# Kernel tuning notes

Hardware: AMD Instinct MI355X
Metric: run time of the kernel (lower is better)

## Reference

```python
import jax, jax.numpy as jnp
import numpy as np

N = 28  # hardcoded grid side in the module


def setup_inputs() -> dict:
    key = jax.random.key(0)
    k1, k2, k3 = jax.random.split(key, 3)
    B = 65536
    x = jax.random.normal(k1, (B, N, N), dtype=jnp.float32)
    # intended init: pos2d = meshgrid positions (xy indexing), stacked on last dim
    xx, yy = jnp.meshgrid(jnp.arange(N), jnp.arange(N), indexing='xy')
    pos2d = jnp.stack([xx, yy], axis=-1).astype(jnp.float32)
    pos2d = pos2d + 0.01 * jax.random.normal(k2, (N, N, 2), dtype=jnp.float32)
    weight = jnp.full((N, N), 0.167, dtype=jnp.float32)
    ep = jnp.full((N, N), -0.1, dtype=jnp.float32) + 0.01 * jax.random.normal(k3, (N, N), dtype=jnp.float32)
    return {"x": x, "pos2d": pos2d, "weight": weight, "ep": ep}


def reference(x, pos2d, weight, ep):
    # grid[a, b] = (b, a) per torch.meshgrid(indexing='xy') stacked on dim -1
    xx, yy = jnp.meshgrid(jnp.arange(N), jnp.arange(N), indexing='xy')
    grid = jnp.stack([xx, yy], axis=-1).astype(pos2d.dtype)            # (28, 28, 2)
    # pairwise position deltas: grid index (a,b) vs learned pos2d at (c,d)
    diff = grid[:, :, None, None, :] - pos2d[None, None, :, :, :]       # (28, 28, 28, 28, 2)
    d2 = jnp.sum(diff * diff, axis=-1)                                  # (28, 28, 28, 28)
    valid = (d2 < 9).astype(d2.dtype)                                   # hard cutoff disk
    ep_neg = -jax.nn.relu(-ep)                                          # clamp ep to <= 0, (28, 28) broadcast over last two dims
    w = jnp.exp(ep_neg * d2) * valid                                    # Gaussian decay * mask
    W = w.reshape(N * N, N * N)                                         # (784, 784)
    B = x.shape[0]
    # torch: matmul(W, x_flat.T).T  ==  x_flat @ W.T
    out = (x.reshape(B, N * N) @ W.T).reshape(B, N, N) * weight
    return out
```

## Files before the change

### kernel.cpp

```cpp
#include <hip/hip_runtime.h>
#include <stdint.h>

typedef __attribute__((ext_vector_type(8))) short short8;
typedef __attribute__((ext_vector_type(4))) float f32x4;
typedef __attribute__((ext_vector_type(8))) float f32x8;
typedef __attribute__((ext_vector_type(16))) float f32x16;
typedef __attribute__((ext_vector_type(2))) float f32x2;
typedef __bf16 bf16x8_t __attribute__((ext_vector_type(8)));

#define NN 784
#define NA 28
#define ABYTES 16384
#define NIMG 128
#define OROW 232

__device__ __forceinline__ unsigned short f2bf(float f) {
  unsigned int u = __float_as_uint(f);
  return (unsigned short)((u + 0x7FFFu + ((u >> 16) & 1u)) >> 16);
}

__device__ __forceinline__ short8 cvt8(f32x4 lo, f32x4 hi) {
  f32x8 f = {lo.x, lo.y, lo.z, lo.w, hi.x, hi.y, hi.z, hi.w};
  bf16x8_t b = __builtin_convertvector(f, bf16x8_t);
  return __builtin_bit_cast(short8, b);
}

__host__ __device__ constexpr int slot0c(int a) {
  int t = 28 * a - 84;
  if (t < 0) t = 0;
  t >>= 5;
  if (t > 17) t = 17;
  return t;
}
__host__ __device__ constexpr int tgtc(int I) { int a2 = I + 2 > 27 ? 27 : I + 2; return slot0c(a2) + 7; }
__host__ __device__ constexpr bool xissue(int I) { return I >= 1 && tgtc(I) > tgtc(I - 1); }
__host__ __device__ constexpr bool xcvt(int A)   { return A >= 3 && xissue(A - 2); }

__global__ void build_w_kernel(const float* __restrict__ pos2d,
                               const float* __restrict__ weight,
                               const float* __restrict__ ep,
                               unsigned short* __restrict__ Bpack) {
  int idx = blockIdx.x * 256 + threadIdx.x;
  int u    = idx & 511;
  int frag = idx >> 9;
  int s2 = frag & 15;
  int a  = frag >> 4;
  int j    = u & 7;
  int lane = u >> 3;
  int outcol = lane & 31;
  int kh     = lane >> 5;
  int kk = kh * 8 + j;
  int kglob = slot0c(a) * 32 + s2 * 16 + kk;
  float val = 0.f;
  if (outcol < 28 && kglob < NN) {
    float px = pos2d[2 * kglob + 0];
    float py = pos2d[2 * kglob + 1];
    float dx = (float)outcol - px;
    float dy = (float)a - py;
    float d2 = __fadd_rn(__fmul_rn(dx, dx), __fmul_rn(dy, dy));
    if (d2 < 9.0f) {
      float en = fminf(ep[kglob], 0.f);
      val = expf(en * d2) * weight[a * 28 + outcol];
    }
  }
  Bpack[idx] = f2bf(val);
}

template <int A>
struct It {
  static __device__ __forceinline__ void run(
      const float* __restrict__ xrow, const unsigned short* __restrict__ Bpack,
      char* __restrict__ wlds, char* __restrict__ olds,
      float* __restrict__ oblk, int tid, int lane,
      short8 (&rlo)[10], short8 (&rhi)[10], f32x4 (&stg)[2][4]) {
    constexpr int T0 = slot0c(A);
    const int il = lane & 31;
    const int kh = lane >> 5;

    f32x4 sr[4];
    if constexpr (A + 1 < NA) {
      const char* src = (const char*)Bpack + (A + 1) * ABYTES + tid * 16;
      #pragma unroll
      for (int r = 0; r < 4; ++r)
        sr[r] = *(const f32x4*)(src + r * 4096);
    }

    if constexpr (xcvt(A)) {
      constexpr int S = slot0c(A) + 7;
      rlo[S % 10] = cvt8(stg[A & 1][0], stg[A & 1][1]);
      if constexpr (S < 24) rhi[S % 10] = cvt8(stg[A & 1][2], stg[A & 1][3]);
      else                  rhi[S % 10] = short8{};
    }
    if constexpr (xissue(A)) {
      constexpr int S = tgtc(A);
      const float* p = xrow + S * 32 + kh * 8;
      stg[A & 1][0] = *(const f32x4*)p;
      stg[A & 1][1] = *(const f32x4*)(p + 4);
      if constexpr (S < 24) {
        stg[A & 1][2] = *(const f32x4*)(p + 16);
        stg[A & 1][3] = *(const f32x4*)(p + 20);
      }
    }

    const char* wbuf = wlds + (A % 3) * ABYTES + lane * 16;
    f32x16 acc = {};
#define KSTEP(s) { constexpr int SL = (T0 + ((s) >> 1)) % 10;                   \
    short8 wf = *(const short8*)(wbuf + (s) * 1024);                            \
    acc = __builtin_amdgcn_mfma_f32_32x32x16_bf16(                              \
        wf, ((s) & 1) ? rhi[SL] : rlo[SL], acc, 0, 0, 0); }
    KSTEP(0)  KSTEP(1)  KSTEP(2)  KSTEP(3)
    KSTEP(4)  KSTEP(5)  KSTEP(6)  KSTEP(7)
    KSTEP(8)  KSTEP(9)  KSTEP(10) KSTEP(11)
    KSTEP(12) KSTEP(13) KSTEP(14) KSTEP(15)
#undef KSTEP

    if constexpr (A + 1 < NA) {
      char* dst = wlds + ((A + 1) % 3) * ABYTES + tid * 16;
      #pragma unroll
      for (int r = 0; r < 4; ++r)
        *(f32x4*)(dst + r * 4096) = sr[r];
    }

    {
      char* obase = olds + (tid >> 6) * 32 * OROW + il * OROW + ((A & 1) * 28 + 4 * kh) * 4;
      #pragma unroll
      for (int g = 0; g < 4; ++g) {
        if (g < 3 || kh == 0) {
          f32x2 v0 = {acc[4 * g + 0], acc[4 * g + 1]};
          f32x2 v1 = {acc[4 * g + 2], acc[4 * g + 3]};
          *(f32x2*)(obase + g * 32) = v0;
          *(f32x2*)(obase + g * 32 + 8) = v1;
        }
      }
    }

    __builtin_amdgcn_s_barrier();

    if constexpr (A & 1) {
      constexpr int P = A >> 1;
      #pragma unroll
      for (int r = 0; r < 14; ++r) {
        int e = r * 256 + tid;
        int img = e / 28, u = e - img * 28;
        f32x2 v = *(const f32x2*)(olds + img * OROW + u * 8);
        *(f32x2*)((char*)(oblk + (size_t)img * NN + P * 56) + u * 8) = v;
      }
      __builtin_amdgcn_s_barrier();
    }

    It<A + 1>::run(xrow, Bpack, wlds, olds, oblk, tid, lane, rlo, rhi, stg);
  }
};
template <>
struct It<NA> {
  static __device__ __forceinline__ void run(const float*, const unsigned short*,
                                             char*, char*, float*, int, int,
                                             short8 (&)[10], short8 (&)[10],
                                             f32x4 (&)[2][4]) {}
};

__global__ __launch_bounds__(256, 2)
void gemm_kernel(const float* __restrict__ x,
                 const unsigned short* __restrict__ Bpack,
                 float* __restrict__ out) {
  __shared__ char wlds[3 * ABYTES];
  __shared__ char olds[NIMG * OROW];

  const int tid  = threadIdx.x;
  const int wave = tid >> 6;
  const int lane = tid & 63;
  const int il   = lane & 31;
  const int kh   = lane >> 5;
  const int m0   = blockIdx.x * NIMG + wave * 32;

  const float* xrow = x + (size_t)(m0 + il) * NN;
  float*       oblk = out + (size_t)(blockIdx.x * NIMG) * NN;

  short8 rlo[10], rhi[10];
  f32x4  stg[2][4];

  {
    const char* src = (const char*)Bpack + tid * 16;
    #pragma unroll
    for (int r = 0; r < 4; ++r) {
      f32x4 v = *(const f32x4*)(src + r * 4096);
      *(f32x4*)(wlds + tid * 16 + r * 4096) = v;
    }
  }

#define PRO(S) { const float* p = xrow + (S) * 32 + kh * 8;                     \
    f32x4 a0 = *(const f32x4*)p,        a1 = *(const f32x4*)(p + 4);            \
    f32x4 b0 = *(const f32x4*)(p + 16), b1 = *(const f32x4*)(p + 20);           \
    rlo[S] = cvt8(a0, a1); rhi[S] = cvt8(b0, b1); }
  PRO(0) PRO(1) PRO(2) PRO(3) PRO(4) PRO(5) PRO(6) PRO(7)
#undef PRO

  __syncthreads();

  It<0>::run(xrow, Bpack, wlds, olds, oblk, tid, lane, rlo, rhi, stg);
}

extern "C" void kernel_launch(void* const* d_in, const int* in_sizes, int n_in,
                              void* d_out, int out_size, void* d_ws, size_t ws_size,
                              hipStream_t stream) {
  const float* x      = (const float*)d_in[0];
  const float* pos2d  = (const float*)d_in[1];
  const float* weight = (const float*)d_in[2];
  const float* ep     = (const float*)d_in[3];
  float* out          = (float*)d_out;
  unsigned short* Bpack = (unsigned short*)d_ws;

  int batch = in_sizes[0] / NN;

  build_w_kernel<<<dim3((NA * 16 * 512) / 256), dim3(256), 0, stream>>>(
      pos2d, weight, ep, Bpack);
  gemm_kernel<<<dim3(batch / NIMG), dim3(256), 0, stream>>>(x, Bpack, out);
}
```

Baseline: 124.4 us.

## Deepen prefetch pipelines and double-buffer output staging to drop extra barriers

The weight-tile prefetch now runs two iterations ahead through a double-buffered register set, and the x-row staging runs three iterations ahead across 12 register slots. Output staging moves to two LDS buffers, each holding one row-block. The store of the previous row-block to global memory is issued before the current block is written to LDS, which removes the second barrier per pair of iterations. MFMA sections also get raised wave priority, and the prologue interleaves loads with conversions. The cost is more live registers under launch_bounds(256,2), which risks spills or lower occupancy.

```diff
diff --git a/kernel.cpp b/kernel.cpp
--- a/kernel.cpp
+++ b/kernel.cpp
@@ -5,14 +5,13 @@
 typedef __attribute__((ext_vector_type(4))) float f32x4;
 typedef __attribute__((ext_vector_type(8))) float f32x8;
 typedef __attribute__((ext_vector_type(16))) float f32x16;
-typedef __attribute__((ext_vector_type(2))) float f32x2;
 typedef __bf16 bf16x8_t __attribute__((ext_vector_type(8)));
 
 #define NN 784
 #define NA 28
 #define ABYTES 16384
 #define NIMG 128
-#define OROW 232
+#define OT 14336
 
 __device__ __forceinline__ unsigned short f2bf(float f) {
   unsigned int u = __float_as_uint(f);
@@ -32,9 +31,9 @@
   if (t > 17) t = 17;
   return t;
 }
-__host__ __device__ constexpr int tgtc(int I) { int a2 = I + 2 > 27 ? 27 : I + 2; return slot0c(a2) + 7; }
-__host__ __device__ constexpr bool xissue(int I) { return I >= 1 && tgtc(I) > tgtc(I - 1); }
-__host__ __device__ constexpr bool xcvt(int A)   { return A >= 3 && xissue(A - 2); }
+__host__ __device__ constexpr int tgt3(int I) { int a2 = I + 3 > 27 ? 27 : I + 3; return slot0c(a2) + 7; }
+__host__ __device__ constexpr bool xiss(int I) { return I >= 1 && tgt3(I) > tgt3(I - 1); }
+__host__ __device__ constexpr bool xcv(int A)  { return A >= 4 && xiss(A - 3); }
 
 __global__ void build_w_kernel(const float* __restrict__ pos2d,
                                const float* __restrict__ weight,
@@ -72,39 +71,39 @@
       const float* __restrict__ xrow, const unsigned short* __restrict__ Bpack,
       char* __restrict__ wlds, char* __restrict__ olds,
       float* __restrict__ oblk, int tid, int lane,
-      short8 (&rlo)[10], short8 (&rhi)[10], f32x4 (&stg)[2][4]) {
+      short8 (&rlo)[12], short8 (&rhi)[12],
+      f32x4 (&stg)[3][4], f32x4 (&sr)[2][4]) {
     constexpr int T0 = slot0c(A);
     const int il = lane & 31;
     const int kh = lane >> 5;
 
-    f32x4 sr[4];
-    if constexpr (A + 1 < NA) {
-      const char* src = (const char*)Bpack + (A + 1) * ABYTES + tid * 16;
+    if constexpr (A + 2 < NA) {
+      const char* src = (const char*)Bpack + (A + 2) * ABYTES + tid * 16;
       #pragma unroll
       for (int r = 0; r < 4; ++r)
-        sr[r] = *(const f32x4*)(src + r * 4096);
-    }
-
-    if constexpr (xcvt(A)) {
-      constexpr int S = slot0c(A) + 7;
-      rlo[S % 10] = cvt8(stg[A & 1][0], stg[A & 1][1]);
-      if constexpr (S < 24) rhi[S % 10] = cvt8(stg[A & 1][2], stg[A & 1][3]);
-      else                  rhi[S % 10] = short8{};
-    }
-    if constexpr (xissue(A)) {
-      constexpr int S = tgtc(A);
+        sr[A & 1][r] = *(const f32x4*)(src + r * 4096);
+    }
+    if constexpr (xcv(A)) {
+      constexpr int S = tgt3(A - 3);
+      rlo[S % 12] = cvt8(stg[A % 3][0], stg[A % 3][1]);
+      if constexpr (S < 24) rhi[S % 12] = cvt8(stg[A % 3][2], stg[A % 3][3]);
+      else                  rhi[S % 12] = short8{};
+    }
+    if constexpr (xiss(A)) {
+      constexpr int S = tgt3(A);
       const float* p = xrow + S * 32 + kh * 8;
-      stg[A & 1][0] = *(const f32x4*)p;
-      stg[A & 1][1] = *(const f32x4*)(p + 4);
+      stg[A % 3][0] = *(const f32x4*)p;
+      stg[A % 3][1] = *(const f32x4*)(p + 4);
       if constexpr (S < 24) {
-        stg[A & 1][2] = *(const f32x4*)(p + 16);
-        stg[A & 1][3] = *(const f32x4*)(p + 20);
+        stg[A % 3][2] = *(const f32x4*)(p + 16);
+        stg[A % 3][3] = *(const f32x4*)(p + 20);
       }
     }
 
     const char* wbuf = wlds + (A % 3) * ABYTES + lane * 16;
     f32x16 acc = {};
-#define KSTEP(s) { constexpr int SL = (T0 + ((s) >> 1)) % 10;                   \
+    __builtin_amdgcn_s_setprio(1);
+#define KSTEP(s) { constexpr int SL = (T0 + ((s) >> 1)) % 12;                   \
     short8 wf = *(const short8*)(wbuf + (s) * 1024);                            \
     acc = __builtin_amdgcn_mfma_f32_32x32x16_bf16(                              \
         wf, ((s) & 1) ? rhi[SL] : rlo[SL], acc, 0, 0, 0); }
@@ -113,91 +112,110 @@
     KSTEP(8)  KSTEP(9)  KSTEP(10) KSTEP(11)
     KSTEP(12) KSTEP(13) KSTEP(14) KSTEP(15)
 #undef KSTEP
+    __builtin_amdgcn_s_setprio(0);
 
     if constexpr (A + 1 < NA) {
       char* dst = wlds + ((A + 1) % 3) * ABYTES + tid * 16;
       #pragma unroll
       for (int r = 0; r < 4; ++r)
-        *(f32x4*)(dst + r * 4096) = sr[r];
-    }
-
-    {
-      char* obase = olds + (tid >> 6) * 32 * OROW + il * OROW + ((A & 1) * 28 + 4 * kh) * 4;
-      #pragma unroll
-      for (int g = 0; g < 4; ++g) {
-        if (g < 3 || kh == 0) {
-          f32x2 v0 = {acc[4 * g + 0], acc[4 * g + 1]};
-          f32x2 v1 = {acc[4 * g + 2], acc[4 * g + 3]};
-          *(f32x2*)(obase + g * 32) = v0;
-          *(f32x2*)(obase + g * 32 + 8) = v1;
+        *(f32x4*)(dst + r * 4096) = sr[(A + 1) & 1][r];
+    }
+
+    if constexpr (A >= 1) {
+      constexpr int P = A - 1;
+      const char* src = olds + (P & 1) * OT;
+      #pragma unroll
+      for (int r = 0; r < 4; ++r) {
+        int e = r * 256 + tid;
+        if (r < 3 || e < 896) {
+          int img = e / 7, u = e - img * 7;
+          f32x4 v = *(const f32x4*)(src + img * 112 + u * 16);
+          *(f32x4*)(oblk + (size_t)img * NN + P * 28 + u * 4) = v;
         }
       }
     }
 
+    {
+      char* ob = olds + (A & 1) * OT + ((tid >> 6) * 32 + il) * 112 + kh * 16;
+      #pragma unroll
+      for (int g = 0; g < 4; ++g)
+        if (g < 3 || kh == 0) {
+          f32x4 v = {acc[4 * g + 0], acc[4 * g + 1], acc[4 * g + 2], acc[4 * g + 3]};
+          *(f32x4*)(ob + g * 32) = v;
+        }
+    }
+
     __builtin_amdgcn_s_barrier();
-
-    if constexpr (A & 1) {
-      constexpr int P = A >> 1;
-      #pragma unroll
-      for (int r = 0; r < 14; ++r) {
-        int e = r * 256 + tid;
-        int img = e / 28, u = e - img * 28;
-        f32x2 v = *(const f32x2*)(olds + img * OROW + u * 8);
-        *(f32x2*)((char*)(oblk + (size_t)img * NN + P * 56) + u * 8) = v;
-      }
-      __builtin_amdgcn_s_barrier();
-    }
-
-    It<A + 1>::run(xrow, Bpack, wlds, olds, oblk, tid, lane, rlo, rhi, stg);
+    It<A + 1>::run(xrow, Bpack, wlds, olds, oblk, tid, lane, rlo, rhi, stg, sr);
   }
 };
 template <>
 struct It<NA> {
   static __device__ __forceinline__ void run(const float*, const unsigned short*,
                                              char*, char*, float*, int, int,
-                                             short8 (&)[10], short8 (&)[10],
-                                             f32x4 (&)[2][4]) {}
+                                             short8 (&)[12], short8 (&)[12],
+                                             f32x4 (&)[3][4], f32x4 (&)[2][4]) {}
 };
 
 __global__ __launch_bounds__(256, 2)
 void gemm_kernel(const float* __restrict__ x,
                  const unsigned short* __restrict__ Bpack,
                  float* __restrict__ out) {
-  __shared__ char wlds[3 * ABYTES];
-  __shared__ char olds[NIMG * OROW];
+  __shared__ __align__(16) char wlds[3 * ABYTES];
+  __shared__ __align__(16) char olds[2 * OT];
 
   const int tid  = threadIdx.x;
   const int wave = tid >> 6;
   const int lane = tid & 63;
   const int il   = lane & 31;
   const int kh   = lane >> 5;
-  const int m0   = blockIdx.x * NIMG + wave * 32;
-
-  const float* xrow = x + (size_t)(m0 + il) * NN;
+
+  const float* xrow = x + (size_t)(blockIdx.x * NIMG + wave * 32 + il) * NN;
   float*       oblk = out + (size_t)(blockIdx.x * NIMG) * NN;
 
-  short8 rlo[10], rhi[10];
-  f32x4  stg[2][4];
+  short8 rlo[12], rhi[12];
+  f32x4  stg[3][4], sr[2][4];
+
+  const char* bsrc = (const char*)Bpack + tid * 16;
+  f32x4 w0r[4];
+  #pragma unroll
+  for (int r = 0; r < 4; ++r)
+    w0r[r] = *(const f32x4*)(bsrc + r * 4096);
+
+#define PLOAD(S) { const float* p = xrow + (S) * 32 + kh * 8;                   \
+    stg[(S) % 3][0] = *(const f32x4*)p;       stg[(S) % 3][1] = *(const f32x4*)(p + 4);  \
+    stg[(S) % 3][2] = *(const f32x4*)(p + 16); stg[(S) % 3][3] = *(const f32x4*)(p + 20); }
+#define PCVT(S)  { rlo[S] = cvt8(stg[(S) % 3][0], stg[(S) % 3][1]);             \
+                   rhi[S] = cvt8(stg[(S) % 3][2], stg[(S) % 3][3]); }
+  PLOAD(0) PLOAD(1) PCVT(0) PLOAD(2) PCVT(1) PLOAD(3) PCVT(2)
+  PLOAD(4) PCVT(3)  PLOAD(5) PCVT(4) PLOAD(6) PCVT(5) PLOAD(7) PCVT(6) PCVT(7)
+#undef PLOAD
+#undef PCVT
+
+  #pragma unroll
+  for (int r = 0; r < 4; ++r)
+    sr[1][r] = *(const f32x4*)(bsrc + ABYTES + r * 4096);
+
+  #pragma unroll
+  for (int r = 0; r < 4; ++r)
+    *(f32x4*)(wlds + tid * 16 + r * 4096) = w0r[r];
+
+  __syncthreads();
+
+  It<0>::run(xrow, Bpack, wlds, olds, oblk, tid, lane, rlo, rhi, stg, sr);
 
   {
-    const char* src = (const char*)Bpack + tid * 16;
+    const char* src = olds + (27 & 1) * OT;
     #pragma unroll
     for (int r = 0; r < 4; ++r) {
-      f32x4 v = *(const f32x4*)(src + r * 4096);
-      *(f32x4*)(wlds + tid * 16 + r * 4096) = v;
+      int e = r * 256 + tid;
+      if (r < 3 || e < 896) {
+        int img = e / 7, u = e - img * 7;
+        f32x4 v = *(const f32x4*)(src + img * 112 + u * 16);
+        *(f32x4*)(oblk + (size_t)img * NN + 27 * 28 + u * 4) = v;
+      }
     }
   }
-
-#define PRO(S) { const float* p = xrow + (S) * 32 + kh * 8;                     \
-    f32x4 a0 = *(const f32x4*)p,        a1 = *(const f32x4*)(p + 4);            \
-    f32x4 b0 = *(const f32x4*)(p + 16), b1 = *(const f32x4*)(p + 20);           \
-    rlo[S] = cvt8(a0, a1); rhi[S] = cvt8(b0, b1); }
-  PRO(0) PRO(1) PRO(2) PRO(3) PRO(4) PRO(5) PRO(6) PRO(7)
-#undef PRO
-
-  __syncthreads();
-
-  It<0>::run(xrow, Bpack, wlds, olds, oblk, tid, lane, rlo, rhi, stg);
 }
 
 extern "C" void kernel_launch(void* const* d_in, const int* in_sizes, int n_in,
```

Measured after the change: 133.8 us. +7.6%, slower.

## Switch to 16x16x32 MFMA with 8 waves of 16 images each

Applied to the files above, without the earlier changes.

Replaces the 32x32x16 bf16 MFMA tiling with pairs of 16x16x32 MFMAs, repacks the weight fragments to match, and halves the per-lane x register ring. Blocks grow from 256 to 512 threads, so each wave handles 16 images instead of 32 while the block still covers 128 images. The aim is to cut register pressure and raise wave occupancy so the streaming x loads and output stores hide better behind compute. In exchange, the block-wide barriers now stall more waves.

```diff
diff --git a/kernel.cpp b/kernel.cpp
--- a/kernel.cpp
+++ b/kernel.cpp
@@ -4,13 +4,14 @@
 typedef __attribute__((ext_vector_type(8))) short short8;
 typedef __attribute__((ext_vector_type(4))) float f32x4;
 typedef __attribute__((ext_vector_type(8))) float f32x8;
-typedef __attribute__((ext_vector_type(16))) float f32x16;
 typedef __attribute__((ext_vector_type(2))) float f32x2;
 typedef __bf16 bf16x8_t __attribute__((ext_vector_type(8)));
 
 #define NN 784
 #define NA 28
-#define ABYTES 16384
+#define NSLOT 8
+#define FRAG_U16 512
+#define ABYTES (NSLOT * 2 * FRAG_U16 * 2)
 #define NIMG 128
 #define OROW 232
 
@@ -43,24 +44,26 @@
   int idx = blockIdx.x * 256 + threadIdx.x;
   int u    = idx & 511;
   int frag = idx >> 9;
-  int s2 = frag & 15;
+  int nf = frag & 1;
+  int s  = (frag >> 1) & 7;
   int a  = frag >> 4;
-  int j    = u & 7;
+  int j8   = u & 7;
   int lane = u >> 3;
-  int outcol = lane & 31;
-  int kh     = lane >> 5;
-  int kk = kh * 8 + j;
-  int kglob = slot0c(a) * 32 + s2 * 16 + kk;
+  int rl = lane & 15;
+  int ch = lane >> 4;
+  int kk = ch * 8 + j8;
+  int kglob = (slot0c(a) + s) * 32 + kk;
+  int ncol  = nf * 16 + rl;
   float val = 0.f;
-  if (outcol < 28 && kglob < NN) {
+  if (ncol < 28 && kglob < NN) {
     float px = pos2d[2 * kglob + 0];
     float py = pos2d[2 * kglob + 1];
-    float dx = (float)outcol - px;
+    float dx = (float)ncol - px;
     float dy = (float)a - py;
     float d2 = __fadd_rn(__fmul_rn(dx, dx), __fmul_rn(dy, dy));
     if (d2 < 9.0f) {
       float en = fminf(ep[kglob], 0.f);
-      val = expf(en * d2) * weight[a * 28 + outcol];
+      val = expf(en * d2) * weight[a * 28 + ncol];
     }
   }
   Bpack[idx] = f2bf(val);
@@ -72,65 +75,54 @@
       const float* __restrict__ xrow, const unsigned short* __restrict__ Bpack,
       char* __restrict__ wlds, char* __restrict__ olds,
       float* __restrict__ oblk, int tid, int lane,
-      short8 (&rlo)[10], short8 (&rhi)[10], f32x4 (&stg)[2][4]) {
+      short8 (&ring)[10], f32x4 (&stg)[2][2]) {
     constexpr int T0 = slot0c(A);
-    const int il = lane & 31;
-    const int kh = lane >> 5;
-
-    f32x4 sr[4];
+    const int rl = lane & 15;
+    const int ch = lane >> 4;
+
+    f32x4 s0, s1;
     if constexpr (A + 1 < NA) {
       const char* src = (const char*)Bpack + (A + 1) * ABYTES + tid * 16;
-      #pragma unroll
-      for (int r = 0; r < 4; ++r)
-        sr[r] = *(const f32x4*)(src + r * 4096);
-    }
-
+      s0 = *(const f32x4*)src;
+      s1 = *(const f32x4*)(src + 8192);
+    }
     if constexpr (xcvt(A)) {
       constexpr int S = slot0c(A) + 7;
-      rlo[S % 10] = cvt8(stg[A & 1][0], stg[A & 1][1]);
-      if constexpr (S < 24) rhi[S % 10] = cvt8(stg[A & 1][2], stg[A & 1][3]);
-      else                  rhi[S % 10] = short8{};
+      if constexpr (S < 24) ring[S % 10] = cvt8(stg[A & 1][0], stg[A & 1][1]);
+      else ring[S % 10] = (ch < 2) ? cvt8(stg[A & 1][0], stg[A & 1][1]) : short8{};
     }
     if constexpr (xissue(A)) {
       constexpr int S = tgtc(A);
-      const float* p = xrow + S * 32 + kh * 8;
+      const float* p = xrow + S * 32 + ((S < 24) ? ch : (ch & 1)) * 8;
       stg[A & 1][0] = *(const f32x4*)p;
       stg[A & 1][1] = *(const f32x4*)(p + 4);
-      if constexpr (S < 24) {
-        stg[A & 1][2] = *(const f32x4*)(p + 16);
-        stg[A & 1][3] = *(const f32x4*)(p + 20);
-      }
     }
 
     const char* wbuf = wlds + (A % 3) * ABYTES + lane * 16;
-    f32x16 acc = {};
-#define KSTEP(s) { constexpr int SL = (T0 + ((s) >> 1)) % 10;                   \
-    short8 wf = *(const short8*)(wbuf + (s) * 1024);                            \
-    acc = __builtin_amdgcn_mfma_f32_32x32x16_bf16(                              \
-        wf, ((s) & 1) ? rhi[SL] : rlo[SL], acc, 0, 0, 0); }
-    KSTEP(0)  KSTEP(1)  KSTEP(2)  KSTEP(3)
-    KSTEP(4)  KSTEP(5)  KSTEP(6)  KSTEP(7)
-    KSTEP(8)  KSTEP(9)  KSTEP(10) KSTEP(11)
-    KSTEP(12) KSTEP(13) KSTEP(14) KSTEP(15)
+    f32x4 acc0 = {}, acc1 = {};
+#define KSTEP(s) { constexpr int SL = (T0 + (s)) % 10;                          \
+    short8 w0 = *(const short8*)(wbuf + ((s) * 2 + 0) * 1024);                  \
+    short8 w1 = *(const short8*)(wbuf + ((s) * 2 + 1) * 1024);                  \
+    acc0 = __builtin_amdgcn_mfma_f32_16x16x32_bf16(w0, ring[SL], acc0, 0, 0, 0);\
+    acc1 = __builtin_amdgcn_mfma_f32_16x16x32_bf16(w1, ring[SL], acc1, 0, 0, 0); }
+    KSTEP(0) KSTEP(1) KSTEP(2) KSTEP(3) KSTEP(4) KSTEP(5) KSTEP(6) KSTEP(7)
 #undef KSTEP
 
     if constexpr (A + 1 < NA) {
       char* dst = wlds + ((A + 1) % 3) * ABYTES + tid * 16;
-      #pragma unroll
-      for (int r = 0; r < 4; ++r)
-        *(f32x4*)(dst + r * 4096) = sr[r];
+      *(f32x4*)dst = s0;
+      *(f32x4*)(dst + 8192) = s1;
     }
 
     {
-      char* obase = olds + (tid >> 6) * 32 * OROW + il * OROW + ((A & 1) * 28 + 4 * kh) * 4;
-      #pragma unroll
-      for (int g = 0; g < 4; ++g) {
-        if (g < 3 || kh == 0) {
-          f32x2 v0 = {acc[4 * g + 0], acc[4 * g + 1]};
-          f32x2 v1 = {acc[4 * g + 2], acc[4 * g + 3]};
-          *(f32x2*)(obase + g * 32) = v0;
-          *(f32x2*)(obase + g * 32 + 8) = v1;
-        }
+      char* ob = olds + ((tid >> 6) * 16 + rl) * OROW + ((A & 1) * 28 + ch * 4) * 4;
+      f32x2 a0lo = {acc0.x, acc0.y}, a0hi = {acc0.z, acc0.w};
+      *(f32x2*)(ob + 0) = a0lo;
+      *(f32x2*)(ob + 8) = a0hi;
+      if (ch < 3) {
+        f32x2 a1lo = {acc1.x, acc1.y}, a1hi = {acc1.z, acc1.w};
+        *(f32x2*)(ob + 64) = a1lo;
+        *(f32x2*)(ob + 72) = a1hi;
       }
     }
 
@@ -139,8 +131,8 @@
     if constexpr (A & 1) {
       constexpr int P = A >> 1;
       #pragma unroll
-      for (int r = 0; r < 14; ++r) {
-        int e = r * 256 + tid;
+      for (int r = 0; r < 7; ++r) {
+        int e = r * 512 + tid;
         int img = e / 28, u = e - img * 28;
         f32x2 v = *(const f32x2*)(olds + img * OROW + u * 8);
         *(f32x2*)((char*)(oblk + (size_t)img * NN + P * 56) + u * 8) = v;
@@ -148,56 +140,52 @@
       __builtin_amdgcn_s_barrier();
     }
 
-    It<A + 1>::run(xrow, Bpack, wlds, olds, oblk, tid, lane, rlo, rhi, stg);
+    It<A + 1>::run(xrow, Bpack, wlds, olds, oblk, tid, lane, ring, stg);
   }
 };
 template <>
 struct It<NA> {
   static __device__ __forceinline__ void run(const float*, const unsigned short*,
                                              char*, char*, float*, int, int,
-                                             short8 (&)[10], short8 (&)[10],
-                                             f32x4 (&)[2][4]) {}
+                                             short8 (&)[10], f32x4 (&)[2][2]) {}
 };
 
-__global__ __launch_bounds__(256, 2)
+__global__ __launch_bounds__(512, 4)
 void gemm_kernel(const float* __restrict__ x,
                  const unsigned short* __restrict__ Bpack,
                  float* __restrict__ out) {
-  __shared__ char wlds[3 * ABYTES];
-  __shared__ char olds[NIMG * OROW];
+  __shared__ __align__(16) char wlds[3 * ABYTES];
+  __shared__ __align__(16) char olds[NIMG * OROW];
 
   const int tid  = threadIdx.x;
   const int wave = tid >> 6;
   const int lane = tid & 63;
-  const int il   = lane & 31;
-  const int kh   = lane >> 5;
-  const int m0   = blockIdx.x * NIMG + wave * 32;
-
-  const float* xrow = x + (size_t)(m0 + il) * NN;
+  const int rl   = lane & 15;
+  const int ch   = lane >> 4;
+
+  const float* xrow = x + (size_t)(blockIdx.x * NIMG + wave * 16 + rl) * NN;
   float*       oblk = out + (size_t)(blockIdx.x * NIMG) * NN;
 
-  short8 rlo[10], rhi[10];
-  f32x4  stg[2][4];
+  short8 ring[10];
+  f32x4  stg[2][2];
 
   {
     const char* src = (const char*)Bpack + tid * 16;
-    #pragma unroll
-    for (int r = 0; r < 4; ++r) {
-      f32x4 v = *(const f32x4*)(src + r * 4096);
-      *(f32x4*)(wlds + tid * 16 + r * 4096) = v;
-    }
+    f32x4 a0 = *(const f32x4*)src;
+    f32x4 a1 = *(const f32x4*)(src + 8192);
+    *(f32x4*)(wlds + tid * 16) = a0;
+    *(f32x4*)(wlds + tid * 16 + 8192) = a1;
   }
 
-#define PRO(S) { const float* p = xrow + (S) * 32 + kh * 8;                     \
-    f32x4 a0 = *(const f32x4*)p,        a1 = *(const f32x4*)(p + 4);            \
-    f32x4 b0 = *(const f32x4*)(p + 16), b1 = *(const f32x4*)(p + 20);           \
-    rlo[S] = cvt8(a0, a1); rhi[S] = cvt8(b0, b1); }
+#define PRO(S) { const float* p = xrow + (S) * 32 + ch * 8;                     \
+    f32x4 lo = *(const f32x4*)p, hi = *(const f32x4*)(p + 4);                   \
+    ring[S] = cvt8(lo, hi); }
   PRO(0) PRO(1) PRO(2) PRO(3) PRO(4) PRO(5) PRO(6) PRO(7)
 #undef PRO
 
   __syncthreads();
 
-  It<0>::run(xrow, Bpack, wlds, olds, oblk, tid, lane, rlo, rhi, stg);
+  It<0>::run(xrow, Bpack, wlds, olds, oblk, tid, lane, ring, stg);
 }
 
 extern "C" void kernel_launch(void* const* d_in, const int* in_sizes, int n_in,
@@ -212,7 +200,7 @@
 
   int batch = in_sizes[0] / NN;
 
-  build_w_kernel<<<dim3((NA * 16 * 512) / 256), dim3(256), 0, stream>>>(
+  build_w_kernel<<<dim3((NA * NSLOT * 2 * FRAG_U16) / 256), dim3(256), 0, stream>>>(
       pos2d, weight, ep, Bpack);
-  gemm_kernel<<<dim3(batch / NIMG), dim3(256), 0, stream>>>(x, Bpack, out);
-}
+  gemm_kernel<<<dim3(batch / NIMG), dim3(512), 0, stream>>>(x, Bpack, out);
+}
```

New measurement: 121.3 us. -2.4%, faster.
